# Optimization experiments

Hardware: AMD Instinct MI355X
Metric: run time of the kernel (lower is better)

The kernel has to match this reference:

```python
import jax, jax.numpy as jnp
import numpy as np

N, F_IN, H = 8192, 256, 64


def setup_inputs() -> dict:
    key = jax.random.key(0)
    ks = jax.random.split(key, 5)
    seq1 = jax.random.normal(ks[0], (1, N, F_IN), jnp.float32)
    seq2 = jax.random.normal(ks[1], (1, N, F_IN), jnp.float32)
    # dense (row-stochastic-ish) adjacency, batch dim 1 as in DGI usage
    adj = jax.random.uniform(ks[2], (1, N, N), jnp.float32) / np.float32(N)
    msk = jnp.ones((1, N), jnp.float32)
    # GCN params: Linear(in_ft, out_ft, bias=False) weight [H, F_IN], bias [H], PReLU alpha
    fc_w = jax.random.normal(ks[3], (H, F_IN), jnp.float32) / np.float32(np.sqrt(F_IN))
    gcn_bias = jnp.zeros((H,), jnp.float32)
    prelu_alpha = jnp.array(0.25, jnp.float32)
    # Discriminator: Bilinear(H, H, 1) -> weight [H, H], bias scalar
    disc_w = jax.random.normal(ks[4], (H, H), jnp.float32) / np.float32(np.sqrt(H))
    disc_b = jnp.zeros((1,), jnp.float32)
    return {"seq1": seq1, "seq2": seq2, "adj": adj, "msk": msk,
            "fc_w": fc_w, "gcn_bias": gcn_bias, "prelu_alpha": prelu_alpha,
            "disc_w": disc_w, "disc_b": disc_b}


def _gcn(seq, adj, fc_w, bias, alpha):
    fts = jnp.einsum('bnf,hf->bnh', seq, fc_w)          # linear, no bias
    out = jnp.einsum('bnm,bmh->bnh', adj, fts) + bias   # dense aggregation + bias
    return jnp.where(out > 0, out, alpha * out)          # PReLU


def reference(seq1, seq2, adj, msk, fc_w, gcn_bias, prelu_alpha, disc_w, disc_b):
    h1 = _gcn(seq1, adj, fc_w, gcn_bias, prelu_alpha)    # [1, N, H]
    # AvgReadout with mask: sum(seq*msk,1)/sum(msk)
    c = jnp.sum(h1 * msk[..., None], axis=1) / jnp.sum(msk)  # [1, H]
    c = jax.nn.sigmoid(c)
    h2 = _gcn(seq2, adj, fc_w, gcn_bias, prelu_alpha)    # [1, N, H]
    # Bilinear discriminator: sc[b,n] = h[b,n,:] @ W @ c[b,:] + b
    wc = jnp.einsum('hk,bk->bh', disc_w, c)              # [1, H]
    sc1 = jnp.einsum('bnh,bh->bn', h1, wc) + disc_b[0]   # [1, N]
    sc2 = jnp.einsum('bnh,bh->bn', h2, wc) + disc_b[0]   # [1, N]
    return jnp.concatenate([sc1, sc2], axis=1)           # [1, 2N]
```

## Files before the change

### kernel.cpp

```cpp
#include <hip/hip_runtime.h>
#include <cstdint>
#include <cstddef>

#define NN 8192
#define FIN 256
#define HH 64
#define SPLIT 16
#define KLEN (NN / SPLIT)

typedef float vf4 __attribute__((ext_vector_type(4)));
typedef short vbf8 __attribute__((ext_vector_type(8)));

__device__ inline unsigned pk_trunc(float lo, float hi) {
  return __builtin_amdgcn_perm(__float_as_uint(hi), __float_as_uint(lo), 0x07060302u);
}
__device__ inline unsigned short bf_rne(float x) {
  unsigned u = __float_as_uint(x);
  return (unsigned short)((u + 0x7FFFu + ((u >> 16) & 1u)) >> 16);
}
__device__ inline float bf_to_f(unsigned short s) {
  return __uint_as_float(((unsigned)s) << 16);
}

union FragU { unsigned u[4]; unsigned short s[8]; vbf8 v; };

__device__ inline vbf8 frag_trunc(vf4 a, vf4 b) {
  FragU t;
  t.u[0] = pk_trunc(a[0], a[1]);
  t.u[1] = pk_trunc(a[2], a[3]);
  t.u[2] = pk_trunc(b[0], b[1]);
  t.u[3] = pk_trunc(b[2], b[3]);
  return t.v;
}
__device__ inline vbf8 frag_rne(vf4 a, vf4 b) {
  FragU t;
  t.s[0] = bf_rne(a[0]); t.s[1] = bf_rne(a[1]); t.s[2] = bf_rne(a[2]); t.s[3] = bf_rne(a[3]);
  t.s[4] = bf_rne(b[0]); t.s[5] = bf_rne(b[1]); t.s[6] = bf_rne(b[2]); t.s[7] = bf_rne(b[3]);
  return t.v;
}

__device__ inline void gl_lds16(const void* g, void* l) {
  __builtin_amdgcn_global_load_lds(
      (const __attribute__((address_space(1))) void*)g,
      (__attribute__((address_space(3))) void*)l, 16, 0, 0);
}

__global__ __launch_bounds__(256) void k1_fts(
    const float* __restrict__ seq1, const float* __restrict__ seq2,
    const float* __restrict__ fcw, unsigned short* __restrict__ Bt,
    float* __restrict__ csum) {
  const int bx = blockIdx.x;
  const int s = bx & 1, mb = bx >> 1;
  const int wave = threadIdx.x >> 6, lane = threadIdx.x & 63;
  const int r = lane & 15, q = lane >> 4;
  const int m0 = mb * 64 + wave * 16;
  if (bx == 0 && threadIdx.x < 64) csum[threadIdx.x] = 0.f;
  const float* seq = s ? seq2 : seq1;
  const float* ap = seq + (size_t)(m0 + r) * FIN + q * 8;
  const float* bp = fcw + (size_t)r * FIN + q * 8;
  vf4 acc[4] = {};
#pragma unroll
  for (int kk = 0; kk < FIN; kk += 32) {
    vf4 a0 = *(const vf4*)ap;
    vf4 a1 = *(const vf4*)(ap + 4);
    vbf8 af = frag_rne(a0, a1);
#pragma unroll
    for (int f = 0; f < 4; ++f) {
      vf4 b0 = *(const vf4*)(bp + (size_t)f * 16 * FIN);
      vf4 b1 = *(const vf4*)(bp + (size_t)f * 16 * FIN + 4);
      vbf8 bfr = frag_rne(b0, b1);
      acc[f] = __builtin_amdgcn_mfma_f32_16x16x32_bf16(af, bfr, acc[f], 0, 0, 0);
    }
    ap += 32; bp += 32;
  }
#pragma unroll
  for (int f = 0; f < 4; ++f) {
    short4 v;
    v.x = (short)bf_rne(acc[f][0]);
    v.y = (short)bf_rne(acc[f][1]);
    v.z = (short)bf_rne(acc[f][2]);
    v.w = (short)bf_rne(acc[f][3]);
    unsigned short* dst = Bt + (size_t)(64 * s + 16 * f + r) * NN + m0 + q * 4;
    *(short4*)dst = v;
  }
}

__global__ __launch_bounds__(512, 4) void k2_agg(
    const float* __restrict__ adj, const unsigned short* __restrict__ Bt,
    unsigned short* __restrict__ Cpart) {
  constexpr int CHUNKS = KLEN / 128;
  __shared__ unsigned short lds[2][16384];
  const int bx = blockIdx.x;
  const int slice = bx & (SPLIT - 1), mb = bx / SPLIT;
  const int wave = threadIdx.x >> 6, lane = threadIdx.x & 63;
  const int r = lane & 15, q = lane >> 4;
  const int m0 = mb * 256 + wave * 32;
  const int k0 = slice * KLEN;

  auto stage = [&](int ch, int b) {
#pragma unroll
    for (int j = 0; j < 4; ++j) {
      const int g = j * 512 + wave * 64 + lane;
      const int r_ = g & 15, q_ = (g >> 4) & 3, f_ = (g >> 6) & 7, kk_ = g >> 9;
      const unsigned short* src =
          Bt + (size_t)(f_ * 16 + r_) * NN + k0 + ch * 128 + kk_ * 32 + q_ * 8;
      gl_lds16(src, &lds[b][(size_t)(j * 512 + wave * 64) * 8]);
    }
  };

  vf4 acc0[8] = {}, acc1[8] = {};
  const float* a0p = adj + (size_t)(m0 + r) * NN + k0 + q * 8;
  const float* a1p = a0p + (size_t)16 * NN;

  stage(0, 0);
  vf4 pa0 = __builtin_nontemporal_load((const vf4*)a0p);
  vf4 pa1 = __builtin_nontemporal_load((const vf4*)a0p + 1);
  vf4 pa2 = __builtin_nontemporal_load((const vf4*)a1p);
  vf4 pa3 = __builtin_nontemporal_load((const vf4*)a1p + 1);

#pragma unroll 1
  for (int ch = 0; ch < CHUNKS; ++ch) {
    const int b = ch & 1;
    asm volatile("s_waitcnt vmcnt(4)" ::: "memory");
    __builtin_amdgcn_s_barrier();
    __builtin_amdgcn_sched_barrier(0);
    if (ch + 1 < CHUNKS) stage(ch + 1, b ^ 1);
    __builtin_amdgcn_sched_barrier(0);
#pragma unroll
    for (int kk = 0; kk < 4; ++kk) {
      const bool more = (kk < 3) || (ch + 1 < CHUNKS);
      const int nc = (kk + 1) * 32;
      vf4 na0, na1, na2, na3;
      if (more) {
        na0 = __builtin_nontemporal_load((const vf4*)(a0p + nc));
        na1 = __builtin_nontemporal_load((const vf4*)(a0p + nc) + 1);
        na2 = __builtin_nontemporal_load((const vf4*)(a1p + nc));
        na3 = __builtin_nontemporal_load((const vf4*)(a1p + nc) + 1);
      }
      vbf8 af0 = frag_trunc(pa0, pa1);
      vbf8 af1 = frag_trunc(pa2, pa3);
#pragma unroll
      for (int f = 0; f < 8; ++f) {
        vbf8 bfr = *(const vbf8*)&lds[b][(size_t)(kk * 512 + f * 64 + lane) * 8];
        acc0[f] = __builtin_amdgcn_mfma_f32_16x16x32_bf16(af0, bfr, acc0[f], 0, 0, 0);
        acc1[f] = __builtin_amdgcn_mfma_f32_16x16x32_bf16(af1, bfr, acc1[f], 0, 0, 0);
      }
      if (more) { pa0 = na0; pa1 = na1; pa2 = na2; pa3 = na3; }
    }
    a0p += 128; a1p += 128;
  }

#pragma unroll
  for (int f = 0; f < 8; ++f) {
    short4 v0, v1;
    v0.x = (short)bf_rne(acc0[f][0]); v0.y = (short)bf_rne(acc0[f][1]);
    v0.z = (short)bf_rne(acc0[f][2]); v0.w = (short)bf_rne(acc0[f][3]);
    v1.x = (short)bf_rne(acc1[f][0]); v1.y = (short)bf_rne(acc1[f][1]);
    v1.z = (short)bf_rne(acc1[f][2]); v1.w = (short)bf_rne(acc1[f][3]);
    unsigned short* d0 = Cpart + ((size_t)slice * 128 + f * 16 + r) * NN + m0 + q * 4;
    *(short4*)d0 = v0;
    *(short4*)(d0 + 16) = v1;
  }
}

__global__ __launch_bounds__(256) void k3a(
    const unsigned short* __restrict__ Cpart, const float* __restrict__ bias,
    const float* __restrict__ alpha_p, const float* __restrict__ msk,
    unsigned short* __restrict__ H, float* __restrict__ csum) {
  const int n = blockIdx.x >> 2, chunk = blockIdx.x & 3;
  const int t = threadIdx.x;
  const int m0 = chunk * 2048 + t * 8;
  const float alpha = alpha_p[0], b = bias[n & 63];
  float v[8] = {};
#pragma unroll
  for (int s = 0; s < SPLIT; ++s) {
    vbf8 c = *(const vbf8*)(Cpart + ((size_t)s * 128 + n) * NN + m0);
#pragma unroll
    for (int j = 0; j < 8; ++j) v[j] += bf_to_f((unsigned short)c[j]);
  }
  FragU hout;
  float acc = 0.f;
#pragma unroll
  for (int j = 0; j < 8; ++j) {
    float x = v[j] + b;
    x = x > 0.f ? x : alpha * x;
    hout.s[j] = bf_rne(x);
    acc += x * msk[m0 + j];
  }
  *(vbf8*)(H + (size_t)n * NN + m0) = hout.v;
  if (n < 64) {
    __shared__ float red[256];
    red[t] = acc;
    __syncthreads();
    for (int off = 128; off > 32; off >>= 1) {
      if (t < off) red[t] += red[t + off];
      __syncthreads();
    }
    if (t < 32) {
      float x = red[t] + red[t + 32];
#pragma unroll
      for (int off = 16; off > 0; off >>= 1) x += __shfl_down(x, off, 64);
      if (t == 0) atomicAdd(&csum[n], x);
    }
  }
}

__global__ __launch_bounds__(256) void k4_sc(
    const unsigned short* __restrict__ H, const float* __restrict__ msk,
    const float* __restrict__ csum, const float* __restrict__ discw,
    const float* __restrict__ discb, float* __restrict__ out) {
  const int t = threadIdx.x, lane = t & 63, w = t >> 6;
  __shared__ float red2[256];
  __shared__ float c_sh[64];
  __shared__ float wc_sh[64];
  float ms = 0.f;
#pragma unroll
  for (int i = 0; i < 32; ++i) ms += msk[t + 256 * i];
  red2[t] = ms;
  __syncthreads();
  for (int off = 128; off > 0; off >>= 1) {
    if (t < off) red2[t] += red2[t + off];
    __syncthreads();
  }
  const float msum = red2[0];
  if (t < 64) c_sh[t] = 1.f / (1.f + __expf(-csum[t] / msum));
  __syncthreads();
  if (t < 64) {
    float wv = 0.f;
#pragma unroll
    for (int k = 0; k < 64; ++k) wv += discw[t * 64 + k] * c_sh[k];
    wc_sh[t] = wv;
  }
  __syncthreads();

  const int m = blockIdx.x * 64 + lane;
  float s = 0.f;
#pragma unroll
  for (int i = 0; i < 32; ++i) {
    const int n = w * 32 + i;
    s += bf_to_f(H[(size_t)n * NN + m]) * wc_sh[n & 63];
  }
  __shared__ float red[4][64];
  red[w][lane] = s;
  __syncthreads();
  if (t < 128) {
    const int half = t >> 6, mm = t & 63;
    out[(size_t)half * NN + blockIdx.x * 64 + mm] =
        red[half * 2][mm] + red[half * 2 + 1][mm] + discb[0];
  }
}

extern "C" void kernel_launch(void* const* d_in, const int* in_sizes, int n_in,
                              void* d_out, int out_size, void* d_ws, size_t ws_size,
                              hipStream_t stream) {
  const float* seq1  = (const float*)d_in[0];
  const float* seq2  = (const float*)d_in[1];
  const float* adj   = (const float*)d_in[2];
  const float* msk   = (const float*)d_in[3];
  const float* fcw   = (const float*)d_in[4];
  const float* bias  = (const float*)d_in[5];
  const float* alpha = (const float*)d_in[6];
  const float* discw = (const float*)d_in[7];
  const float* discb = (const float*)d_in[8];
  float* out = (float*)d_out;
  char* ws = (char*)d_ws;

  unsigned short* Bt    = (unsigned short*)ws;
  unsigned short* Cpart = (unsigned short*)(ws + (size_t)(2 << 20));
  unsigned short* H     = (unsigned short*)(ws + (size_t)(34 << 20));
  float* csum           = (float*)(ws + (size_t)(36 << 20));

  hipLaunchKernelGGL(k1_fts, dim3(256), dim3(256), 0, stream, seq1, seq2, fcw, Bt, csum);
  hipLaunchKernelGGL(k2_agg, dim3(32 * SPLIT), dim3(512), 0, stream, adj, Bt, Cpart);
  hipLaunchKernelGGL(k3a, dim3(512), dim3(256), 0, stream, Cpart, bias, alpha, msk, H, csum);
  hipLaunchKernelGGL(k4_sc, dim3(128), dim3(256), 0, stream, H, msk, csum, discw, discb, out);
}
```

Measured before the change: 426.7 us.

## Halve split-K and per-wave row tile in aggregation kernel, drop adj prefetch

Reduces the split-K factor from 16 to 8 and gives each wave a single 16-row MFMA tile instead of two. The grid is kept at 512 blocks, each covering 128 rows over a longer K range. The manual register double-buffering of adjacency loads and the hand-placed vmcnt/barrier are replaced by plain per-step loads and __syncthreads. This halves the partial-sum buffer written and then re-read by the reduction kernel, at the cost of half the LDS B-fragment reuse per wave and less latency hiding on the dominant adjacency stream.

```diff
diff --git a/kernel.cpp b/kernel.cpp
--- a/kernel.cpp
+++ b/kernel.cpp
@@ -5,7 +5,7 @@
 #define NN 8192
 #define FIN 256
 #define HH 64
-#define SPLIT 16
+#define SPLIT 8
 #define KLEN (NN / SPLIT)
 
 typedef float vf4 __attribute__((ext_vector_type(4)));
@@ -94,7 +94,7 @@
   const int slice = bx & (SPLIT - 1), mb = bx / SPLIT;
   const int wave = threadIdx.x >> 6, lane = threadIdx.x & 63;
   const int r = lane & 15, q = lane >> 4;
-  const int m0 = mb * 256 + wave * 32;
+  const int m0 = mb * 128 + wave * 16;
   const int k0 = slice * KLEN;
 
   auto stage = [&](int ch, int b) {
@@ -108,58 +108,36 @@
     }
   };
 
-  vf4 acc0[8] = {}, acc1[8] = {};
-  const float* a0p = adj + (size_t)(m0 + r) * NN + k0 + q * 8;
-  const float* a1p = a0p + (size_t)16 * NN;
+  vf4 acc[8] = {};
+  const float* ap = adj + (size_t)(m0 + r) * NN + k0 + q * 8;
 
   stage(0, 0);
-  vf4 pa0 = __builtin_nontemporal_load((const vf4*)a0p);
-  vf4 pa1 = __builtin_nontemporal_load((const vf4*)a0p + 1);
-  vf4 pa2 = __builtin_nontemporal_load((const vf4*)a1p);
-  vf4 pa3 = __builtin_nontemporal_load((const vf4*)a1p + 1);
-
 #pragma unroll 1
   for (int ch = 0; ch < CHUNKS; ++ch) {
+    __syncthreads();
+    if (ch + 1 < CHUNKS) stage(ch + 1, (ch + 1) & 1);
     const int b = ch & 1;
-    asm volatile("s_waitcnt vmcnt(4)" ::: "memory");
-    __builtin_amdgcn_s_barrier();
-    __builtin_amdgcn_sched_barrier(0);
-    if (ch + 1 < CHUNKS) stage(ch + 1, b ^ 1);
-    __builtin_amdgcn_sched_barrier(0);
 #pragma unroll
     for (int kk = 0; kk < 4; ++kk) {
-      const bool more = (kk < 3) || (ch + 1 < CHUNKS);
-      const int nc = (kk + 1) * 32;
-      vf4 na0, na1, na2, na3;
-      if (more) {
-        na0 = __builtin_nontemporal_load((const vf4*)(a0p + nc));
-        na1 = __builtin_nontemporal_load((const vf4*)(a0p + nc) + 1);
-        na2 = __builtin_nontemporal_load((const vf4*)(a1p + nc));
-        na3 = __builtin_nontemporal_load((const vf4*)(a1p + nc) + 1);
-      }
-      vbf8 af0 = frag_trunc(pa0, pa1);
-      vbf8 af1 = frag_trunc(pa2, pa3);
+      const int kc = ch * 128 + kk * 32;
+      vf4 a0 = __builtin_nontemporal_load((const vf4*)(ap + kc));
+      vf4 a1 = __builtin_nontemporal_load((const vf4*)(ap + kc) + 1);
+      vbf8 af = frag_trunc(a0, a1);
 #pragma unroll
       for (int f = 0; f < 8; ++f) {
         vbf8 bfr = *(const vbf8*)&lds[b][(size_t)(kk * 512 + f * 64 + lane) * 8];
-        acc0[f] = __builtin_amdgcn_mfma_f32_16x16x32_bf16(af0, bfr, acc0[f], 0, 0, 0);
-        acc1[f] = __builtin_amdgcn_mfma_f32_16x16x32_bf16(af1, bfr, acc1[f], 0, 0, 0);
+        acc[f] = __builtin_amdgcn_mfma_f32_16x16x32_bf16(af, bfr, acc[f], 0, 0, 0);
       }
-      if (more) { pa0 = na0; pa1 = na1; pa2 = na2; pa3 = na3; }
-    }
-    a0p += 128; a1p += 128;
+    }
   }
 
 #pragma unroll
   for (int f = 0; f < 8; ++f) {
-    short4 v0, v1;
-    v0.x = (short)bf_rne(acc0[f][0]); v0.y = (short)bf_rne(acc0[f][1]);
-    v0.z = (short)bf_rne(acc0[f][2]); v0.w = (short)bf_rne(acc0[f][3]);
-    v1.x = (short)bf_rne(acc1[f][0]); v1.y = (short)bf_rne(acc1[f][1]);
-    v1.z = (short)bf_rne(acc1[f][2]); v1.w = (short)bf_rne(acc1[f][3]);
+    short4 v;
+    v.x = (short)bf_rne(acc[f][0]); v.y = (short)bf_rne(acc[f][1]);
+    v.z = (short)bf_rne(acc[f][2]); v.w = (short)bf_rne(acc[f][3]);
     unsigned short* d0 = Cpart + ((size_t)slice * 128 + f * 16 + r) * NN + m0 + q * 4;
-    *(short4*)d0 = v0;
-    *(short4*)(d0 + 16) = v1;
+    *(short4*)d0 = v;
   }
 }
 
@@ -267,11 +245,11 @@
 
   unsigned short* Bt    = (unsigned short*)ws;
   unsigned short* Cpart = (unsigned short*)(ws + (size_t)(2 << 20));
-  unsigned short* H     = (unsigned short*)(ws + (size_t)(34 << 20));
-  float* csum           = (float*)(ws + (size_t)(36 << 20));
+  unsigned short* H     = (unsigned short*)(ws + (size_t)(18 << 20));
+  float* csum           = (float*)(ws + (size_t)(20 << 20));
 
   hipLaunchKernelGGL(k1_fts, dim3(256), dim3(256), 0, stream, seq1, seq2, fcw, Bt, csum);
-  hipLaunchKernelGGL(k2_agg, dim3(32 * SPLIT), dim3(512), 0, stream, adj, Bt, Cpart);
+  hipLaunchKernelGGL(k2_agg, dim3(64 * SPLIT), dim3(512), 0, stream, adj, Bt, Cpart);
   hipLaunchKernelGGL(k3a, dim3(512), dim3(256), 0, stream, Cpart, bias, alpha, msk, H, csum);
   hipLaunchKernelGGL(k4_sc, dim3(128), dim3(256), 0, stream, H, msk, csum, discw, discb, out);
 }
```

After: 402.5 us. -5.7%, faster.
